# Kernel tuning notes

Hardware: AMD Instinct MI355X
Metric: run time of the kernel (lower is better)

## Reference

```python
import jax, jax.numpy as jnp
import numpy as np

N_NODES = 50000
N_EDGES = 600000
IN_FEATS = 128
N_HIDDEN = 128
N_CLASSES = 40


def setup_inputs() -> dict:
    key = jax.random.key(0)
    ks = jax.random.split(key, 12)
    feat = jax.random.normal(ks[0], (N_NODES, IN_FEATS), dtype=jnp.float32)
    src = jax.random.randint(ks[1], (N_EDGES,), 0, N_NODES, dtype=jnp.int32)
    dst = jax.random.randint(ks[2], (N_EDGES,), 0, N_NODES, dtype=jnp.int32)
    dims = [(IN_FEATS, N_HIDDEN), (N_HIDDEN, N_HIDDEN), (N_HIDDEN, N_CLASSES)]
    params = {}
    for i, (di, do) in enumerate(dims):
        s = 1.0 / np.sqrt(di)
        params[f"w_self{i}"] = jax.random.uniform(ks[3 + 3 * i], (di, do), jnp.float32, -s, s)
        params[f"w_neigh{i}"] = jax.random.uniform(ks[4 + 3 * i], (di, do), jnp.float32, -s, s)
        params[f"b{i}"] = jnp.zeros((do,), jnp.float32)
    return dict(feat=feat, src=src, dst=dst, **params)


def _sage_layer(h, src, dst, w_self, w_neigh, b):
    # mean aggregation over in-neighbors: msg = h[src], reduce at dst
    msg_sum = jax.ops.segment_sum(h[src], dst, num_segments=N_NODES)  # [N, d]
    deg = jax.ops.segment_sum(jnp.ones((src.shape[0],), h.dtype), dst, num_segments=N_NODES)
    h_neigh = msg_sum / jnp.maximum(deg, 1.0)[:, None]
    # DGL SAGEConv(mean): out = fc_self(h) + fc_neigh(mean_neigh) + bias
    return h @ w_self + h_neigh @ w_neigh + b


def reference(feat, src, dst,
              w_self0, w_neigh0, b0,
              w_self1, w_neigh1, b1,
              w_self2, w_neigh2, b2):
    # dropout p=0.0 -> identity
    h = _sage_layer(feat, src, dst, w_self0, w_neigh0, b0)
    h = jax.nn.relu(h)
    h = _sage_layer(h, src, dst, w_self1, w_neigh1, b1)
    h = jax.nn.relu(h)
    h = _sage_layer(h, src, dst, w_self2, w_neigh2, b2)
    return h
```

## Files before the change

kernel.cpp:

```cpp
#include <hip/hip_runtime.h>

#define N_NODES 50000
#define N_EDGES 600000
#define NBLK    196
#define KDIM    128
#define APAD    136

typedef short bf16x8 __attribute__((ext_vector_type(8)));
typedef float f32x4  __attribute__((ext_vector_type(4)));
typedef unsigned short u16x8 __attribute__((ext_vector_type(8)));
typedef unsigned short u16x4 __attribute__((ext_vector_type(4)));

__device__ inline ushort rne_bf16(float a) {
    union { float f; unsigned u; } v; v.f = a;
    return (ushort)((v.u + 0x7FFFu + ((v.u >> 16) & 1u)) >> 16);
}
__device__ inline float bf16_to_f32(ushort h) {
    return __uint_as_float((unsigned)h << 16);
}
__device__ inline void split_bf16(float a, ushort& hi, ushort& lo) {
    hi = rne_bf16(a);
    float hv = bf16_to_f32(hi);
    lo = rne_bf16(a - hv);
}

__global__ __launch_bounds__(256) void k_prep(
    const int* __restrict__ dst, int* __restrict__ degi,
    const float* __restrict__ ws0, const float* __restrict__ wn0,
    const float* __restrict__ ws1, const float* __restrict__ wn1,
    const float* __restrict__ ws2, const float* __restrict__ wn2,
    ushort* __restrict__ Bth0, ushort* __restrict__ Btl0,
    ushort* __restrict__ Bth1, ushort* __restrict__ Btl1,
    ushort* __restrict__ Bth2, ushort* __restrict__ Btl2)
{
    const int b = blockIdx.x, t = threadIdx.x;
    if (b < 192) {
        for (int e = b * 256 + t; e < N_EDGES; e += 192 * 256)
            atomicAdd(&degi[dst[e]], 1);
    } else {
        for (int i = (b - 192) * 256 + t; i < 592 * 128; i += 64 * 256) {
            int bb = i >> 7, k = i & 127;
            const float *Ws, *Wn;
            ushort *H, *L;
            int dout, n;
            if (bb < 256)      { n = bb;       dout = 128; Ws = ws0; Wn = wn0; H = Bth0; L = Btl0; }
            else if (bb < 512) { n = bb - 256; dout = 128; Ws = ws1; Wn = wn1; H = Bth1; L = Btl1; }
            else               { n = bb - 512; dout = 40;  Ws = ws2; Wn = wn2; H = Bth2; L = Btl2; }
            float w = (n < dout) ? Ws[(long)k * dout + n] : Wn[(long)k * dout + (n - dout)];
            ushort hi, lo;
            split_bf16(w, hi, lo);
            H[n * 128 + k] = hi;
            L[n * 128 + k] = lo;
        }
    }
}

__global__ __launch_bounds__(256) void block_sums_kernel(const int* __restrict__ deg,
                                                         int* __restrict__ bsum, int n) {
    __shared__ int s[256];
    int t = threadIdx.x;
    int i = blockIdx.x * 256 + t;
    s[t] = (i < n) ? deg[i] : 0;
    __syncthreads();
    #pragma unroll
    for (int d = 128; d > 0; d >>= 1) {
        if (t < d) s[t] += s[t + d];
        __syncthreads();
    }
    if (t == 0) bsum[blockIdx.x] = s[0];
}

__global__ __launch_bounds__(256) void scatter_fused_kernel(const int* __restrict__ deg,
                                                            const int* __restrict__ bsum,
                                                            int* __restrict__ off,
                                                            int* __restrict__ cur,
                                                            int n, int nb) {
    __shared__ int s[256];
    int t = threadIdx.x;

    int bv = (t < nb) ? bsum[t] : 0;
    s[t] = bv;
    __syncthreads();
    #pragma unroll
    for (int d = 1; d < 256; d <<= 1) {
        int x = (t >= d) ? s[t - d] : 0;
        __syncthreads();
        s[t] += x;
        __syncthreads();
    }
    int base = (blockIdx.x > 0) ? s[blockIdx.x - 1] : 0;
    if (blockIdx.x == 0 && t == 0) off[n] = s[255];
    __syncthreads();

    int i = blockIdx.x * 256 + t;
    int v = (i < n) ? deg[i] : 0;
    s[t] = v;
    __syncthreads();
    #pragma unroll
    for (int d = 1; d < 256; d <<= 1) {
        int x = (t >= d) ? s[t - d] : 0;
        __syncthreads();
        s[t] += x;
        __syncthreads();
    }
    if (i < n) {
        int excl = s[t] - v + base;
        off[i] = excl;
        cur[i] = excl;
    }
}

__device__ __forceinline__ void load_a16(const float* __restrict__ A, int grow, int M, int seg,
                                         float* __restrict__ f) {
    if (grow < M) {
        const float* ap = A + (long)grow * KDIM + seg;
        #pragma unroll
        for (int q = 0; q < 4; ++q) {
            float4 a = *(const float4*)(ap + q * 4);
            f[q * 4 + 0] = a.x; f[q * 4 + 1] = a.y;
            f[q * 4 + 2] = a.z; f[q * 4 + 3] = a.w;
        }
    } else {
        #pragma unroll
        for (int i = 0; i < 16; ++i) f[i] = 0.f;
    }
}

__device__ __forceinline__ void split_store16(const float* __restrict__ f,
                                              ushort* __restrict__ Ahi, ushort* __restrict__ Alo,
                                              int m, int seg) {
    ushort h[16], l[16];
    #pragma unroll
    for (int i = 0; i < 16; ++i) split_bf16(f[i], h[i], l[i]);
    #pragma unroll
    for (int q = 0; q < 2; ++q) {
        uint4 hw, lw;
        hw.x = (unsigned)h[q*8+0] | ((unsigned)h[q*8+1] << 16);
        hw.y = (unsigned)h[q*8+2] | ((unsigned)h[q*8+3] << 16);
        hw.z = (unsigned)h[q*8+4] | ((unsigned)h[q*8+5] << 16);
        hw.w = (unsigned)h[q*8+6] | ((unsigned)h[q*8+7] << 16);
        lw.x = (unsigned)l[q*8+0] | ((unsigned)l[q*8+1] << 16);
        lw.y = (unsigned)l[q*8+2] | ((unsigned)l[q*8+3] << 16);
        lw.z = (unsigned)l[q*8+4] | ((unsigned)l[q*8+5] << 16);
        lw.w = (unsigned)l[q*8+6] | ((unsigned)l[q*8+7] << 16);
        *(uint4*)&Ahi[m * APAD + seg + q * 8] = hw;
        *(uint4*)&Alo[m * APAD + seg + q * 8] = lw;
    }
}

__device__ __forceinline__ void load_pl(const ushort* __restrict__ Phi, const ushort* __restrict__ Plo,
                                        int grow, int M, int seg, uint4* __restrict__ r) {
    if (grow < M) {
        const uint4* ph = (const uint4*)(Phi + (long)grow * KDIM + seg);
        const uint4* pl = (const uint4*)(Plo + (long)grow * KDIM + seg);
        r[0] = ph[0]; r[1] = ph[1];
        r[2] = pl[0]; r[3] = pl[1];
    } else {
        uint4 z = {0, 0, 0, 0};
        r[0] = r[1] = r[2] = r[3] = z;
    }
}

__device__ __forceinline__ void store_pl(const uint4* __restrict__ r,
                                         ushort* __restrict__ Ahi, ushort* __restrict__ Alo,
                                         int m, int seg) {
    *(uint4*)&Ahi[m * APAD + seg] = r[0];
    *(uint4*)&Ahi[m * APAD + seg + 8] = r[1];
    *(uint4*)&Alo[m * APAD + seg] = r[2];
    *(uint4*)&Alo[m * APAD + seg + 8] = r[3];
}

#define WIDE_MFMA_TILE()                                                                      \
    f32x4 acc[2][2] = {};                                                                     \
    _Pragma("unroll")                                                                         \
    for (int c = 0; c < 4; ++c) {                                                             \
        const int k0 = c * 32 + quad * 8;                                                     \
        bf16x8 ah[2], al[2];                                                                  \
        _Pragma("unroll")                                                                     \
        for (int r = 0; r < 2; ++r) {                                                         \
            const int off = (16 * r + lane16) * APAD + k0;                                    \
            ah[r] = *(const bf16x8*)&AH[off];                                                 \
            al[r] = *(const bf16x8*)&AL[off];                                                 \
        }                                                                                     \
        _Pragma("unroll")                                                                     \
        for (int ct = 0; ct < 2; ++ct) {                                                      \
            _Pragma("unroll")                                                                 \
            for (int r = 0; r < 2; ++r) {                                                     \
                acc[r][ct] = __builtin_amdgcn_mfma_f32_16x16x32_bf16(Bh[c][ct], ah[r], acc[r][ct], 0, 0, 0); \
                acc[r][ct] = __builtin_amdgcn_mfma_f32_16x16x32_bf16(Bl[c][ct], ah[r], acc[r][ct], 0, 0, 0); \
                acc[r][ct] = __builtin_amdgcn_mfma_f32_16x16x32_bf16(Bh[c][ct], al[r], acc[r][ct], 0, 0, 0); \
            }                                                                                 \
        }                                                                                     \
    }

#define WIDE_STORE_TILE()                                                                     \
    _Pragma("unroll")                                                                         \
    for (int ct = 0; ct < 2; ++ct) {                                                          \
        const int colL = wave * 32 + 16 * ct + quad * 4;                                      \
        _Pragma("unroll")                                                                     \
        for (int r = 0; r < 2; ++r) {                                                         \
            const int row = rt * 32 + 16 * r + lane16;                                        \
            if (row < M) {                                                                    \
                if (half == 0) {                                                              \
                    *(f32x4*)(S + (long)row * 128 + colL) = acc[r][ct] + bv[ct];              \
                } else {                                                                      \
                    u16x4 t4;                                                                 \
                    _Pragma("unroll")                                                         \
                    for (int i = 0; i < 4; ++i) t4[i] = rne_bf16(acc[r][ct][i]);              \
                    *(u16x4*)(T + (long)row * 128 + colL) = t4;                               \
                }                                                                             \
            }                                                                                 \
        }                                                                                     \
    }

#define WIDE_B_PROLOGUE()                                                                     \
    bf16x8 Bh[4][2], Bl[4][2];                                                                \
    _Pragma("unroll")                                                                         \
    for (int c = 0; c < 4; ++c) {                                                             \
        _Pragma("unroll")                                                                     \
        for (int ct = 0; ct < 2; ++ct) {                                                      \
            const long boff = (long)(colbase + 16 * ct + lane16) * KDIM + c * 32 + quad * 8;  \
            Bh[c][ct] = *(const bf16x8*)(Bth + boff);                                         \
            Bl[c][ct] = *(const bf16x8*)(Btl + boff);                                         \
        }                                                                                     \
    }                                                                                         \
    f32x4 bv[2] = {};                                                                         \
    if (half == 0) {                                                                          \
        _Pragma("unroll")                                                                     \
        for (int ct = 0; ct < 2; ++ct)                                                        \
            bv[ct] = *(const f32x4*)(bias + wave * 32 + 16 * ct + quad * 4);                  \
    }

__global__ __launch_bounds__(256, 3) void k_gemm_wide_f32_fill(
    const float* __restrict__ A,
    const ushort* __restrict__ Bth, const ushort* __restrict__ Btl,
    const float* __restrict__ bias,
    float* __restrict__ S, ushort* __restrict__ T, int M,
    const int* __restrict__ src, const int* __restrict__ dst,
    int* __restrict__ cur, int* __restrict__ ssrcb)
{
    __shared__ ushort AhiB[2][32 * APAD];
    __shared__ ushort AloB[2][32 * APAD];

    if (blockIdx.x < 128) {
        const int gtid = blockIdx.x * 256 + threadIdx.x;
        for (int e = gtid; e < N_EDGES; e += 128 * 256) {
            int p = atomicAdd(&cur[dst[e]], 1);
            ssrcb[p] = src[e];
        }
        return;
    }

    const int bid = blockIdx.x - 128;
    const int tid = threadIdx.x;
    const int wave = tid >> 6;
    const int lane = tid & 63;
    const int lane16 = lane & 15;
    const int quad = lane >> 4;
    const int half = bid & 1;
    const int colbase = half * 128 + wave * 32;
    const int ntiles = (M + 31) >> 5;
    const int bstride = 320;
    const int m   = tid >> 3;
    const int seg = (tid & 7) * 16;

    WIDE_B_PROLOGUE();

    int rt = bid >> 1;
    if (rt >= ntiles) return;

    float fa[16];
    load_a16(A, rt * 32 + m, M, seg, fa);
    split_store16(fa, &AhiB[0][0], &AloB[0][0], m, seg);
    __syncthreads();

    int cur_b = 0;
    while (true) {
        const int nrt = rt + bstride;
        float fn[16];
        if (nrt < ntiles) load_a16(A, nrt * 32 + m, M, seg, fn);

        const ushort* AH = &AhiB[cur_b][0];
        const ushort* AL = &AloB[cur_b][0];

        WIDE_MFMA_TILE();
        WIDE_STORE_TILE();

        if (nrt >= ntiles) break;
        split_store16(fn, &AhiB[cur_b ^ 1][0], &AloB[cur_b ^ 1][0], m, seg);
        __syncthreads();
        cur_b ^= 1;
        rt = nrt;
    }
}

__global__ __launch_bounds__(256, 3) void k_gemm_wide_pl(
    const ushort* __restrict__ Phi, const ushort* __restrict__ Plo,
    const ushort* __restrict__ Bth, const ushort* __restrict__ Btl,
    const float* __restrict__ bias,
    float* __restrict__ S, ushort* __restrict__ T, int M)
{
    __shared__ ushort AhiB[2][32 * APAD];
    __shared__ ushort AloB[2][32 * APAD];

    const int tid = threadIdx.x;
    const int wave = tid >> 6;
    const int lane = tid & 63;
    const int lane16 = lane & 15;
    const int quad = lane >> 4;
    const int half = blockIdx.x & 1;
    const int colbase = half * 128 + wave * 32;
    const int ntiles = (M + 31) >> 5;
    const int bstride = gridDim.x >> 1;
    const int m   = tid >> 3;
    const int seg = (tid & 7) * 16;

    WIDE_B_PROLOGUE();

    int rt = blockIdx.x >> 1;
    if (rt >= ntiles) return;

    uint4 ra[4];
    load_pl(Phi, Plo, rt * 32 + m, M, seg, ra);
    store_pl(ra, &AhiB[0][0], &AloB[0][0], m, seg);
    __syncthreads();

    int cur_b = 0;
    while (true) {
        const int nrt = rt + bstride;
        uint4 rn[4];
        if (nrt < ntiles) load_pl(Phi, Plo, nrt * 32 + m, M, seg, rn);

        const ushort* AH = &AhiB[cur_b][0];
        const ushort* AL = &AloB[cur_b][0];

        WIDE_MFMA_TILE();
        WIDE_STORE_TILE();

        if (nrt >= ntiles) break;
        store_pl(rn, &AhiB[cur_b ^ 1][0], &AloB[cur_b ^ 1][0], m, seg);
        __syncthreads();
        cur_b ^= 1;
        rt = nrt;
    }
}

__global__ __launch_bounds__(256, 2) void k_gemm_narrow_pl(
    const ushort* __restrict__ Phi, const ushort* __restrict__ Plo,
    const ushort* __restrict__ Bth, const ushort* __restrict__ Btl,
    const float* __restrict__ bias,
    float* __restrict__ S, ushort* __restrict__ T, int M)
{
    __shared__ ushort AhiB[2][32 * APAD];
    __shared__ ushort AloB[2][32 * APAD];

    const int tid = threadIdx.x;
    const int wave = tid >> 6;
    const int lane = tid & 63;
    const int lane16 = lane & 15;
    const int quad = lane >> 4;
    const int rtw = wave & 1;
    const int cg = wave >> 1;
    const int ctbase = cg * 3;
    const int nct = cg ? 2 : 3;
    const int ntiles = (M + 31) >> 5;
    const int m   = tid >> 3;
    const int seg = (tid & 7) * 16;

    bf16x8 Bh[4][3], Bl[4][3];
    #pragma unroll
    for (int c = 0; c < 4; ++c) {
        #pragma unroll
        for (int j = 0; j < 3; ++j) {
            if (j < nct) {
                const long boff = (long)(16 * (ctbase + j) + lane16) * KDIM + c * 32 + quad * 8;
                Bh[c][j] = *(const bf16x8*)(Bth + boff);
                Bl[c][j] = *(const bf16x8*)(Btl + boff);
            }
        }
    }

    int rt = blockIdx.x;
    if (rt >= ntiles) return;

    uint4 ra[4];
    load_pl(Phi, Plo, rt * 32 + m, M, seg, ra);
    store_pl(ra, &AhiB[0][0], &AloB[0][0], m, seg);
    __syncthreads();

    int cur_b = 0;
    while (true) {
        const int nrt = rt + gridDim.x;
        uint4 rn[4];
        if (nrt < ntiles) load_pl(Phi, Plo, nrt * 32 + m, M, seg, rn);

        const ushort* AH = &AhiB[cur_b][0];
        const ushort* AL = &AloB[cur_b][0];

        f32x4 acc[3] = {};
        #pragma unroll
        for (int c = 0; c < 4; ++c) {
            const int off = (rtw * 16 + lane16) * APAD + c * 32 + quad * 8;
            bf16x8 ah = *(const bf16x8*)&AH[off];
            bf16x8 al = *(const bf16x8*)&AL[off];
            #pragma unroll
            for (int j = 0; j < 3; ++j) {
                if (j < nct) {
                    acc[j] = __builtin_amdgcn_mfma_f32_16x16x32_bf16(Bh[c][j], ah, acc[j], 0, 0, 0);
                    acc[j] = __builtin_amdgcn_mfma_f32_16x16x32_bf16(Bl[c][j], ah, acc[j], 0, 0, 0);
                    acc[j] = __builtin_amdgcn_mfma_f32_16x16x32_bf16(Bh[c][j], al, acc[j], 0, 0, 0);
                }
            }
        }

        const int row = rt * 32 + rtw * 16 + lane16;
        #pragma unroll
        for (int j = 0; j < 3; ++j) {
            if (j < nct && row < M) {
                const int col0 = 16 * (ctbase + j) + quad * 4;
                if (col0 < 40) {
                    f32x4 bvv = *(const f32x4*)(bias + col0);
                    *(f32x4*)(S + (long)row * 40 + col0) = acc[j] + bvv;
                } else {
                    u16x4 t4;
                    #pragma unroll
                    for (int i = 0; i < 4; ++i) t4[i] = rne_bf16(acc[j][i]);
                    *(u16x4*)(T + (long)row * 40 + (col0 - 40)) = t4;
                }
            }
        }

        if (nrt >= ntiles) break;
        store_pl(rn, &AhiB[cur_b ^ 1][0], &AloB[cur_b ^ 1][0], m, seg);
        __syncthreads();
        cur_b ^= 1;
        rt = nrt;
    }
}

__global__ __launch_bounds__(256) void k_agg128_pl(
    const float* __restrict__ S, const ushort* __restrict__ T,
    const int* __restrict__ off, const int* __restrict__ ssrcb,
    ushort* __restrict__ Phi, ushort* __restrict__ Plo, int nnodes)
{
    const int node = (blockIdx.x * 256 + threadIdx.x) >> 6;
    if (node >= nnodes) return;
    const int lane = threadIdx.x & 63;
    const int slot = lane >> 4;
    const int col8 = (lane & 15) * 8;

    const int a = off[node];
    const int b = off[node + 1];

    f32x4 acc0a = {0,0,0,0}, acc0b = {0,0,0,0};
    f32x4 acc1a = {0,0,0,0}, acc1b = {0,0,0,0};

    int i = a;
    for (; i + 8 <= b; i += 8) {
        int s0 = ssrcb[i + slot];
        int s1 = ssrcb[i + 4 + slot];
        u16x8 v0 = *(const u16x8*)(T + (long)s0 * 128 + col8);
        u16x8 v1 = *(const u16x8*)(T + (long)s1 * 128 + col8);
        #pragma unroll
        for (int j = 0; j < 4; ++j) {
            acc0a[j] += bf16_to_f32(v0[j]);
            acc0b[j] += bf16_to_f32(v0[4 + j]);
            acc1a[j] += bf16_to_f32(v1[j]);
            acc1b[j] += bf16_to_f32(v1[4 + j]);
        }
    }
    for (; i < b; i += 4) {
        int e = i + slot;
        if (e < b) {
            int s = ssrcb[e];
            u16x8 v = *(const u16x8*)(T + (long)s * 128 + col8);
            #pragma unroll
            for (int j = 0; j < 4; ++j) {
                acc0a[j] += bf16_to_f32(v[j]);
                acc0b[j] += bf16_to_f32(v[4 + j]);
            }
        }
    }
    f32x4 accA = acc0a + acc1a;
    f32x4 accB = acc0b + acc1b;

    #pragma unroll
    for (int mm = 16; mm <= 32; mm <<= 1) {
        #pragma unroll
        for (int j = 0; j < 4; ++j) {
            accA[j] += __shfl_xor((float)accA[j], mm);
            accB[j] += __shfl_xor((float)accB[j], mm);
        }
    }

    if (slot == 0) {
        int deg = b - a;
        float scale = (deg > 0) ? (1.0f / (float)deg) : 0.f;
        f32x4 sA = *(const f32x4*)(S + (long)node * 128 + col8);
        f32x4 sB = *(const f32x4*)(S + (long)node * 128 + col8 + 4);
        f32x4 rA = sA + accA * scale;
        f32x4 rB = sB + accB * scale;
        #pragma unroll
        for (int j = 0; j < 4; ++j) {
            rA[j] = fmaxf(rA[j], 0.f);
            rB[j] = fmaxf(rB[j], 0.f);
        }
        u16x8 ph, pl;
        #pragma unroll
        for (int j = 0; j < 4; ++j) {
            ushort h, l;
            split_bf16(rA[j], h, l); ph[j] = h; pl[j] = l;
        }
        #pragma unroll
        for (int j = 0; j < 4; ++j) {
            ushort h, l;
            split_bf16(rB[j], h, l); ph[4 + j] = h; pl[4 + j] = l;
        }
        *(u16x8*)(Phi + (long)node * 128 + col8) = ph;
        *(u16x8*)(Plo + (long)node * 128 + col8) = pl;
    }
}

__global__ __launch_bounds__(256) void k_agg40(
    const float* __restrict__ S, const ushort* __restrict__ T,
    const int* __restrict__ off, const int* __restrict__ ssrcb,
    float* __restrict__ out, int nnodes)
{
    const int node = (blockIdx.x * 256 + threadIdx.x) >> 6;
    if (node >= nnodes) return;
    const int lane = threadIdx.x & 63;
    const bool active = lane < 60;
    const int slot = active ? (lane / 10) : 5;
    const int fi = lane % 10;
    const int fo = fi * 4;

    const int a = off[node];
    const int b = off[node + 1];

    f32x4 acc0 = {0,0,0,0}, acc1 = {0,0,0,0};

    int i = a;
    for (; i + 12 <= b; i += 12) {
        int s0 = ssrcb[i + slot];
        int s1 = ssrcb[i + 6 + slot];
        u16x4 v0 = *(const u16x4*)(T + (long)s0 * 40 + fo);
        u16x4 v1 = *(const u16x4*)(T + (long)s1 * 40 + fo);
        if (active) {
            #pragma unroll
            for (int j = 0; j < 4; ++j) {
                acc0[j] += bf16_to_f32(v0[j]);
                acc1[j] += bf16_to_f32(v1[j]);
            }
        }
    }
    for (; i < b; i += 6) {
        int e = i + slot;
        if (active && e < b) {
            int s = ssrcb[e];
            u16x4 v = *(const u16x4*)(T + (long)s * 40 + fo);
            #pragma unroll
            for (int j = 0; j < 4; ++j) acc0[j] += bf16_to_f32(v[j]);
        }
    }
    f32x4 acc = acc0 + acc1;

    f32x4 tot = acc;
    #pragma unroll
    for (int d = 10; d <= 50; d += 10) {
        int srcl = fi + d;
        #pragma unroll
        for (int j = 0; j < 4; ++j) tot[j] += __shfl((float)acc[j], srcl);
    }

    if (lane < 10) {
        int deg = b - a;
        float scale = (deg > 0) ? (1.0f / (float)deg) : 0.f;
        f32x4 s4 = *(const f32x4*)(S + (long)node * 40 + fo);
        f32x4 r = s4 + tot * scale;
        *(f32x4*)(out + (long)node * 40 + fo) = r;
    }
}


extern "C" void kernel_launch(void* const* d_in, const int* in_sizes, int n_in,
                              void* d_out, int out_size, void* d_ws, size_t ws_size,
                              hipStream_t stream) {
    const float* feat = (const float*)d_in[0];
    const int*   src  = (const int*)d_in[1];
    const int*   dst  = (const int*)d_in[2];
    const float* ws0  = (const float*)d_in[3];
    const float* wn0  = (const float*)d_in[4];
    const float* b0   = (const float*)d_in[5];
    const float* ws1  = (const float*)d_in[6];
    const float* wn1  = (const float*)d_in[7];
    const float* b1   = (const float*)d_in[8];
    const float* ws2  = (const float*)d_in[9];
    const float* wn2  = (const float*)d_in[10];
    const float* b2   = (const float*)d_in[11];

    const int N = N_NODES;

    char* ws = (char*)d_ws;
    int*    offsets = (int*)(ws + 0);
    int*    cursor  = (int*)(ws + 200704);
    int*    degi    = (int*)(ws + 401408);
    int*    bsum    = (int*)(ws + 601600);
    int*    ssrcb   = (int*)(ws + 603648);
    ushort* Phi  = (ushort*)(ws + 3003904);
    ushort* Plo  = (ushort*)(ws + 15803904);
    float*  sbuf = (float*)(ws + 28603904);
    ushort* tbuf = (ushort*)(ws + 54203904);

    ushort* Ball = (ushort*)d_out;
    ushort* Bth0 = Ball;
    ushort* Btl0 = Ball + 32768;
    ushort* Bth1 = Ball + 65536;
    ushort* Btl1 = Ball + 98304;
    ushort* Bth2 = Ball + 131072;
    ushort* Btl2 = Ball + 141312;

    hipMemsetAsync(degi, 0, (size_t)N * sizeof(int), stream);
    k_prep<<<256, 256, 0, stream>>>(dst, degi, ws0, wn0, ws1, wn1, ws2, wn2,
                                    Bth0, Btl0, Bth1, Btl1, Bth2, Btl2);

    block_sums_kernel<<<NBLK, 256, 0, stream>>>(degi, bsum, N);
    scatter_fused_kernel<<<NBLK, 256, 0, stream>>>(degi, bsum, offsets, cursor, N, NBLK);

    const int ga = (N + 3) / 4;

    k_gemm_wide_f32_fill<<<768, 256, 0, stream>>>(feat, Bth0, Btl0, b0, sbuf, tbuf, N,
                                                  src, dst, cursor, ssrcb);
    k_agg128_pl<<<ga, 256, 0, stream>>>(sbuf, tbuf, offsets, ssrcb, Phi, Plo, N);

    k_gemm_wide_pl<<<768, 256, 0, stream>>>(Phi, Plo, Bth1, Btl1, b1, sbuf, tbuf, N);
    k_agg128_pl<<<ga, 256, 0, stream>>>(sbuf, tbuf, offsets, ssrcb, Phi, Plo, N);

    k_gemm_narrow_pl<<<512, 256, 0, stream>>>(Phi, Plo, Bth2, Btl2, b2, sbuf, tbuf, N);
    k_agg40<<<ga, 256, 0, stream>>>(sbuf, tbuf, offsets, ssrcb, (float*)d_out, N);
}
```

Baseline: 275.9 us.

## Drop LDS staging in GEMMs; pre-split input features into bf16 hi/lo in prep

The GEMM kernels no longer stage A tiles through double-buffered shared memory. Each wave now loads its bf16 hi/lo fragments directly from global memory, with the last row clamped for out-of-range tiles. The fp32 input features are split into bf16 hi/lo once in the prep kernel, which grows to 768 blocks, so the first GEMM reads the same hi/lo format as the later layers. This removes LDS traffic, barriers and the in-GEMM split and allows higher occupancy hints. The cost is redundant global or L2 reads across waves that share rows, and an extra pass writing the split features.

```diff
diff --git a/kernel.cpp b/kernel.cpp
--- a/kernel.cpp
+++ b/kernel.cpp
@@ -4,7 +4,6 @@
 #define N_EDGES 600000
 #define NBLK    196
 #define KDIM    128
-#define APAD    136
 
 typedef short bf16x8 __attribute__((ext_vector_type(8)));
 typedef float f32x4  __attribute__((ext_vector_type(4)));
@@ -26,6 +25,8 @@
 
 __global__ __launch_bounds__(256) void k_prep(
     const int* __restrict__ dst, int* __restrict__ degi,
+    const float* __restrict__ feat,
+    ushort* __restrict__ Fhi, ushort* __restrict__ Flo,
     const float* __restrict__ ws0, const float* __restrict__ wn0,
     const float* __restrict__ ws1, const float* __restrict__ wn1,
     const float* __restrict__ ws2, const float* __restrict__ wn2,
@@ -37,7 +38,7 @@
     if (b < 192) {
         for (int e = b * 256 + t; e < N_EDGES; e += 192 * 256)
             atomicAdd(&degi[dst[e]], 1);
-    } else {
+    } else if (b < 256) {
         for (int i = (b - 192) * 256 + t; i < 592 * 128; i += 64 * 256) {
             int bb = i >> 7, k = i & 127;
             const float *Ws, *Wn;
@@ -52,6 +53,35 @@
             H[n * 128 + k] = hi;
             L[n * 128 + k] = lo;
         }
+    } else {
+        for (int idx = (b - 256) * 256 + t; idx < N_NODES * 8; idx += 512 * 256) {
+            const int row = idx >> 3;
+            const int seg = (idx & 7) * 16;
+            const float* ap = feat + (long)row * KDIM + seg;
+            float f[16];
+            #pragma unroll
+            for (int q = 0; q < 4; ++q) {
+                float4 a = *(const float4*)(ap + q * 4);
+                f[q*4+0] = a.x; f[q*4+1] = a.y; f[q*4+2] = a.z; f[q*4+3] = a.w;
+            }
+            ushort h[16], l[16];
+            #pragma unroll
+            for (int i = 0; i < 16; ++i) split_bf16(f[i], h[i], l[i]);
+            #pragma unroll
+            for (int q = 0; q < 2; ++q) {
+                uint4 hw, lw;
+                hw.x = (unsigned)h[q*8+0] | ((unsigned)h[q*8+1] << 16);
+                hw.y = (unsigned)h[q*8+2] | ((unsigned)h[q*8+3] << 16);
+                hw.z = (unsigned)h[q*8+4] | ((unsigned)h[q*8+5] << 16);
+                hw.w = (unsigned)h[q*8+6] | ((unsigned)h[q*8+7] << 16);
+                lw.x = (unsigned)l[q*8+0] | ((unsigned)l[q*8+1] << 16);
+                lw.y = (unsigned)l[q*8+2] | ((unsigned)l[q*8+3] << 16);
+                lw.z = (unsigned)l[q*8+4] | ((unsigned)l[q*8+5] << 16);
+                lw.w = (unsigned)l[q*8+6] | ((unsigned)l[q*8+7] << 16);
+                *(uint4*)&Fhi[(long)row * KDIM + seg + q * 8] = hw;
+                *(uint4*)&Flo[(long)row * KDIM + seg + q * 8] = lw;
+            }
+        }
     }
 }
 
@@ -110,90 +140,47 @@
     }
 }
 
-__device__ __forceinline__ void load_a16(const float* __restrict__ A, int grow, int M, int seg,
-                                         float* __restrict__ f) {
-    if (grow < M) {
-        const float* ap = A + (long)grow * KDIM + seg;
-        #pragma unroll
-        for (int q = 0; q < 4; ++q) {
-            float4 a = *(const float4*)(ap + q * 4);
-            f[q * 4 + 0] = a.x; f[q * 4 + 1] = a.y;
-            f[q * 4 + 2] = a.z; f[q * 4 + 3] = a.w;
-        }
-    } else {
-        #pragma unroll
-        for (int i = 0; i < 16; ++i) f[i] = 0.f;
-    }
-}
-
-__device__ __forceinline__ void split_store16(const float* __restrict__ f,
-                                              ushort* __restrict__ Ahi, ushort* __restrict__ Alo,
-                                              int m, int seg) {
-    ushort h[16], l[16];
-    #pragma unroll
-    for (int i = 0; i < 16; ++i) split_bf16(f[i], h[i], l[i]);
-    #pragma unroll
-    for (int q = 0; q < 2; ++q) {
-        uint4 hw, lw;
-        hw.x = (unsigned)h[q*8+0] | ((unsigned)h[q*8+1] << 16);
-        hw.y = (unsigned)h[q*8+2] | ((unsigned)h[q*8+3] << 16);
-        hw.z = (unsigned)h[q*8+4] | ((unsigned)h[q*8+5] << 16);
-        hw.w = (unsigned)h[q*8+6] | ((unsigned)h[q*8+7] << 16);
-        lw.x = (unsigned)l[q*8+0] | ((unsigned)l[q*8+1] << 16);
-        lw.y = (unsigned)l[q*8+2] | ((unsigned)l[q*8+3] << 16);
-        lw.z = (unsigned)l[q*8+4] | ((unsigned)l[q*8+5] << 16);
-        lw.w = (unsigned)l[q*8+6] | ((unsigned)l[q*8+7] << 16);
-        *(uint4*)&Ahi[m * APAD + seg + q * 8] = hw;
-        *(uint4*)&Alo[m * APAD + seg + q * 8] = lw;
-    }
-}
-
-__device__ __forceinline__ void load_pl(const ushort* __restrict__ Phi, const ushort* __restrict__ Plo,
-                                        int grow, int M, int seg, uint4* __restrict__ r) {
-    if (grow < M) {
-        const uint4* ph = (const uint4*)(Phi + (long)grow * KDIM + seg);
-        const uint4* pl = (const uint4*)(Plo + (long)grow * KDIM + seg);
-        r[0] = ph[0]; r[1] = ph[1];
-        r[2] = pl[0]; r[3] = pl[1];
-    } else {
-        uint4 z = {0, 0, 0, 0};
-        r[0] = r[1] = r[2] = r[3] = z;
-    }
-}
-
-__device__ __forceinline__ void store_pl(const uint4* __restrict__ r,
-                                         ushort* __restrict__ Ahi, ushort* __restrict__ Alo,
-                                         int m, int seg) {
-    *(uint4*)&Ahi[m * APAD + seg] = r[0];
-    *(uint4*)&Ahi[m * APAD + seg + 8] = r[1];
-    *(uint4*)&Alo[m * APAD + seg] = r[2];
-    *(uint4*)&Alo[m * APAD + seg + 8] = r[3];
-}
-
-#define WIDE_MFMA_TILE()                                                                      \
+
+#define WIDE_B_PROLOGUE()                                                                     \
+    bf16x8 Bh[4][2], Bl[4][2];                                                                \
+    _Pragma("unroll")                                                                         \
+    for (int c = 0; c < 4; ++c) {                                                             \
+        _Pragma("unroll")                                                                     \
+        for (int ct = 0; ct < 2; ++ct) {                                                      \
+            const long boff = (long)(colbase + 16 * ct + lane16) * KDIM + c * 32 + quad * 8;  \
+            Bh[c][ct] = *(const bf16x8*)(Bth + boff);                                         \
+            Bl[c][ct] = *(const bf16x8*)(Btl + boff);                                         \
+        }                                                                                     \
+    }                                                                                         \
+    f32x4 bv[2] = {};                                                                         \
+    if (half == 0) {                                                                          \
+        _Pragma("unroll")                                                                     \
+        for (int ct = 0; ct < 2; ++ct)                                                        \
+            bv[ct] = *(const f32x4*)(bias + wave * 32 + 16 * ct + quad * 4);                  \
+    }
+
+#define WIDE_TILE_BODY()                                                                      \
+    const int rr0 = rt * 32 + lane16;                                                         \
+    const int rr1 = rr0 + 16;                                                                 \
+    const long ro0 = (long)((rr0 < M) ? rr0 : (M - 1)) * KDIM + quad * 8;                     \
+    const long ro1 = (long)((rr1 < M) ? rr1 : (M - 1)) * KDIM + quad * 8;                     \
     f32x4 acc[2][2] = {};                                                                     \
     _Pragma("unroll")                                                                         \
     for (int c = 0; c < 4; ++c) {                                                             \
-        const int k0 = c * 32 + quad * 8;                                                     \
-        bf16x8 ah[2], al[2];                                                                  \
-        _Pragma("unroll")                                                                     \
-        for (int r = 0; r < 2; ++r) {                                                         \
-            const int off = (16 * r + lane16) * APAD + k0;                                    \
-            ah[r] = *(const bf16x8*)&AH[off];                                                 \
-            al[r] = *(const bf16x8*)&AL[off];                                                 \
-        }                                                                                     \
+        bf16x8 ah0 = *(const bf16x8*)(Phi + ro0 + c * 32);                                    \
+        bf16x8 al0 = *(const bf16x8*)(Plo + ro0 + c * 32);                                    \
+        bf16x8 ah1 = *(const bf16x8*)(Phi + ro1 + c * 32);                                    \
+        bf16x8 al1 = *(const bf16x8*)(Plo + ro1 + c * 32);                                    \
         _Pragma("unroll")                                                                     \
         for (int ct = 0; ct < 2; ++ct) {                                                      \
-            _Pragma("unroll")                                                                 \
-            for (int r = 0; r < 2; ++r) {                                                     \
-                acc[r][ct] = __builtin_amdgcn_mfma_f32_16x16x32_bf16(Bh[c][ct], ah[r], acc[r][ct], 0, 0, 0); \
-                acc[r][ct] = __builtin_amdgcn_mfma_f32_16x16x32_bf16(Bl[c][ct], ah[r], acc[r][ct], 0, 0, 0); \
-                acc[r][ct] = __builtin_amdgcn_mfma_f32_16x16x32_bf16(Bh[c][ct], al[r], acc[r][ct], 0, 0, 0); \
-            }                                                                                 \
+            acc[0][ct] = __builtin_amdgcn_mfma_f32_16x16x32_bf16(Bh[c][ct], ah0, acc[0][ct], 0, 0, 0); \
+            acc[0][ct] = __builtin_amdgcn_mfma_f32_16x16x32_bf16(Bl[c][ct], ah0, acc[0][ct], 0, 0, 0); \
+            acc[0][ct] = __builtin_amdgcn_mfma_f32_16x16x32_bf16(Bh[c][ct], al0, acc[0][ct], 0, 0, 0); \
+            acc[1][ct] = __builtin_amdgcn_mfma_f32_16x16x32_bf16(Bh[c][ct], ah1, acc[1][ct], 0, 0, 0); \
+            acc[1][ct] = __builtin_amdgcn_mfma_f32_16x16x32_bf16(Bl[c][ct], ah1, acc[1][ct], 0, 0, 0); \
+            acc[1][ct] = __builtin_amdgcn_mfma_f32_16x16x32_bf16(Bh[c][ct], al1, acc[1][ct], 0, 0, 0); \
         }                                                                                     \
-    }
-
-#define WIDE_STORE_TILE()                                                                     \
+    }                                                                                         \
     _Pragma("unroll")                                                                         \
     for (int ct = 0; ct < 2; ++ct) {                                                          \
         const int colL = wave * 32 + 16 * ct + quad * 4;                                      \
@@ -213,35 +200,14 @@
         }                                                                                     \
     }
 
-#define WIDE_B_PROLOGUE()                                                                     \
-    bf16x8 Bh[4][2], Bl[4][2];                                                                \
-    _Pragma("unroll")                                                                         \
-    for (int c = 0; c < 4; ++c) {                                                             \
-        _Pragma("unroll")                                                                     \
-        for (int ct = 0; ct < 2; ++ct) {                                                      \
-            const long boff = (long)(colbase + 16 * ct + lane16) * KDIM + c * 32 + quad * 8;  \
-            Bh[c][ct] = *(const bf16x8*)(Bth + boff);                                         \
-            Bl[c][ct] = *(const bf16x8*)(Btl + boff);                                         \
-        }                                                                                     \
-    }                                                                                         \
-    f32x4 bv[2] = {};                                                                         \
-    if (half == 0) {                                                                          \
-        _Pragma("unroll")                                                                     \
-        for (int ct = 0; ct < 2; ++ct)                                                        \
-            bv[ct] = *(const f32x4*)(bias + wave * 32 + 16 * ct + quad * 4);                  \
-    }
-
-__global__ __launch_bounds__(256, 3) void k_gemm_wide_f32_fill(
-    const float* __restrict__ A,
+__global__ __launch_bounds__(256, 4) void k_gemm_wide_pl_fill(
+    const ushort* __restrict__ Phi, const ushort* __restrict__ Plo,
     const ushort* __restrict__ Bth, const ushort* __restrict__ Btl,
     const float* __restrict__ bias,
     float* __restrict__ S, ushort* __restrict__ T, int M,
     const int* __restrict__ src, const int* __restrict__ dst,
     int* __restrict__ cur, int* __restrict__ ssrcb)
 {
-    __shared__ ushort AhiB[2][32 * APAD];
-    __shared__ ushort AloB[2][32 * APAD];
-
     if (blockIdx.x < 128) {
         const int gtid = blockIdx.x * 256 + threadIdx.x;
         for (int e = gtid; e < N_EDGES; e += 128 * 256) {
@@ -260,49 +226,20 @@
     const int half = bid & 1;
     const int colbase = half * 128 + wave * 32;
     const int ntiles = (M + 31) >> 5;
-    const int bstride = 320;
-    const int m   = tid >> 3;
-    const int seg = (tid & 7) * 16;
 
     WIDE_B_PROLOGUE();
 
-    int rt = bid >> 1;
-    if (rt >= ntiles) return;
-
-    float fa[16];
-    load_a16(A, rt * 32 + m, M, seg, fa);
-    split_store16(fa, &AhiB[0][0], &AloB[0][0], m, seg);
-    __syncthreads();
-
-    int cur_b = 0;
-    while (true) {
-        const int nrt = rt + bstride;
-        float fn[16];
-        if (nrt < ntiles) load_a16(A, nrt * 32 + m, M, seg, fn);
-
-        const ushort* AH = &AhiB[cur_b][0];
-        const ushort* AL = &AloB[cur_b][0];
-
-        WIDE_MFMA_TILE();
-        WIDE_STORE_TILE();
-
-        if (nrt >= ntiles) break;
-        split_store16(fn, &AhiB[cur_b ^ 1][0], &AloB[cur_b ^ 1][0], m, seg);
-        __syncthreads();
-        cur_b ^= 1;
-        rt = nrt;
-    }
-}
-
-__global__ __launch_bounds__(256, 3) void k_gemm_wide_pl(
+    for (int rt = bid >> 1; rt < ntiles; rt += 320) {
+        WIDE_TILE_BODY();
+    }
+}
+
+__global__ __launch_bounds__(256, 4) void k_gemm_wide_pl(
     const ushort* __restrict__ Phi, const ushort* __restrict__ Plo,
     const ushort* __restrict__ Bth, const ushort* __restrict__ Btl,
     const float* __restrict__ bias,
     float* __restrict__ S, ushort* __restrict__ T, int M)
 {
-    __shared__ ushort AhiB[2][32 * APAD];
-    __shared__ ushort AloB[2][32 * APAD];
-
     const int tid = threadIdx.x;
     const int wave = tid >> 6;
     const int lane = tid & 63;
@@ -312,48 +249,20 @@
     const int colbase = half * 128 + wave * 32;
     const int ntiles = (M + 31) >> 5;
     const int bstride = gridDim.x >> 1;
-    const int m   = tid >> 3;
-    const int seg = (tid & 7) * 16;
 
     WIDE_B_PROLOGUE();
 
-    int rt = blockIdx.x >> 1;
-    if (rt >= ntiles) return;
-
-    uint4 ra[4];
-    load_pl(Phi, Plo, rt * 32 + m, M, seg, ra);
-    store_pl(ra, &AhiB[0][0], &AloB[0][0], m, seg);
-    __syncthreads();
-
-    int cur_b = 0;
-    while (true) {
-        const int nrt = rt + bstride;
-        uint4 rn[4];
-        if (nrt < ntiles) load_pl(Phi, Plo, nrt * 32 + m, M, seg, rn);
-
-        const ushort* AH = &AhiB[cur_b][0];
-        const ushort* AL = &AloB[cur_b][0];
-
-        WIDE_MFMA_TILE();
-        WIDE_STORE_TILE();
-
-        if (nrt >= ntiles) break;
-        store_pl(rn, &AhiB[cur_b ^ 1][0], &AloB[cur_b ^ 1][0], m, seg);
-        __syncthreads();
-        cur_b ^= 1;
-        rt = nrt;
-    }
-}
-
-__global__ __launch_bounds__(256, 2) void k_gemm_narrow_pl(
+    for (int rt = blockIdx.x >> 1; rt < ntiles; rt += bstride) {
+        WIDE_TILE_BODY();
+    }
+}
+
+__global__ __launch_bounds__(256, 3) void k_gemm_narrow_pl(
     const ushort* __restrict__ Phi, const ushort* __restrict__ Plo,
     const ushort* __restrict__ Bth, const ushort* __restrict__ Btl,
     const float* __restrict__ bias,
     float* __restrict__ S, ushort* __restrict__ T, int M)
 {
-    __shared__ ushort AhiB[2][32 * APAD];
-    __shared__ ushort AloB[2][32 * APAD];
-
     const int tid = threadIdx.x;
     const int wave = tid >> 6;
     const int lane = tid & 63;
@@ -364,8 +273,6 @@
     const int ctbase = cg * 3;
     const int nct = cg ? 2 : 3;
     const int ntiles = (M + 31) >> 5;
-    const int m   = tid >> 3;
-    const int seg = (tid & 7) * 16;
 
     bf16x8 Bh[4][3], Bl[4][3];
     #pragma unroll
@@ -380,29 +287,15 @@
         }
     }
 
-    int rt = blockIdx.x;
-    if (rt >= ntiles) return;
-
-    uint4 ra[4];
-    load_pl(Phi, Plo, rt * 32 + m, M, seg, ra);
-    store_pl(ra, &AhiB[0][0], &AloB[0][0], m, seg);
-    __syncthreads();
-
-    int cur_b = 0;
-    while (true) {
-        const int nrt = rt + gridDim.x;
-        uint4 rn[4];
-        if (nrt < ntiles) load_pl(Phi, Plo, nrt * 32 + m, M, seg, rn);
-
-        const ushort* AH = &AhiB[cur_b][0];
-        const ushort* AL = &AloB[cur_b][0];
+    for (int rt = blockIdx.x; rt < ntiles; rt += gridDim.x) {
+        const int rr = rt * 32 + rtw * 16 + lane16;
+        const long ro = (long)((rr < M) ? rr : (M - 1)) * KDIM + quad * 8;
 
         f32x4 acc[3] = {};
         #pragma unroll
         for (int c = 0; c < 4; ++c) {
-            const int off = (rtw * 16 + lane16) * APAD + c * 32 + quad * 8;
-            bf16x8 ah = *(const bf16x8*)&AH[off];
-            bf16x8 al = *(const bf16x8*)&AL[off];
+            bf16x8 ah = *(const bf16x8*)(Phi + ro + c * 32);
+            bf16x8 al = *(const bf16x8*)(Plo + ro + c * 32);
             #pragma unroll
             for (int j = 0; j < 3; ++j) {
                 if (j < nct) {
@@ -429,12 +322,6 @@
                 }
             }
         }
-
-        if (nrt >= ntiles) break;
-        store_pl(rn, &AhiB[cur_b ^ 1][0], &AloB[cur_b ^ 1][0], m, seg);
-        __syncthreads();
-        cur_b ^= 1;
-        rt = nrt;
     }
 }
 
@@ -620,7 +507,8 @@
     ushort* Btl2 = Ball + 141312;
 
     hipMemsetAsync(degi, 0, (size_t)N * sizeof(int), stream);
-    k_prep<<<256, 256, 0, stream>>>(dst, degi, ws0, wn0, ws1, wn1, ws2, wn2,
+    k_prep<<<768, 256, 0, stream>>>(dst, degi, feat, Phi, Plo,
+                                    ws0, wn0, ws1, wn1, ws2, wn2,
                                     Bth0, Btl0, Bth1, Btl1, Bth2, Btl2);
 
     block_sums_kernel<<<NBLK, 256, 0, stream>>>(degi, bsum, N);
@@ -628,8 +516,8 @@
 
     const int ga = (N + 3) / 4;
 
-    k_gemm_wide_f32_fill<<<768, 256, 0, stream>>>(feat, Bth0, Btl0, b0, sbuf, tbuf, N,
-                                                  src, dst, cursor, ssrcb);
+    k_gemm_wide_pl_fill<<<768, 256, 0, stream>>>(Phi, Plo, Bth0, Btl0, b0, sbuf, tbuf, N,
+                                                 src, dst, cursor, ssrcb);
     k_agg128_pl<<<ga, 256, 0, stream>>>(sbuf, tbuf, offsets, ssrcb, Phi, Plo, N);
 
     k_gemm_wide_pl<<<768, 256, 0, stream>>>(Phi, Plo, Bth1, Btl1, b1, sbuf, tbuf, N);
```

Result: slower. 302.0 us (+9.4%).

## Use atomic work-stealing tile counters in the three GEMM kernels

Applied to the files above, without the earlier changes.

Replaces the static grid-stride row-tile assignment in the wide and narrow GEMM kernels with dynamic tile fetching from global atomic counters (one per column half), prefetched one tile ahead through a double-buffered shared slot. The goal is to balance load across blocks, especially in the fused fill kernel where edge-scatter blocks compete for the GPU with GEMM blocks. The counters live in workspace and are zeroed by extending the existing memset. The cost is one extra atomic and a shared-memory broadcast per tile, and consecutive tiles may now land on different blocks, which changes cache locality.

```diff
diff --git a/kernel.cpp b/kernel.cpp
--- a/kernel.cpp
+++ b/kernel.cpp
@@ -237,10 +237,12 @@
     const float* __restrict__ bias,
     float* __restrict__ S, ushort* __restrict__ T, int M,
     const int* __restrict__ src, const int* __restrict__ dst,
-    int* __restrict__ cur, int* __restrict__ ssrcb)
+    int* __restrict__ cur, int* __restrict__ ssrcb,
+    int* __restrict__ ctr)
 {
     __shared__ ushort AhiB[2][32 * APAD];
     __shared__ ushort AloB[2][32 * APAD];
+    __shared__ int s_tile[2];
 
     if (blockIdx.x < 128) {
         const int gtid = blockIdx.x * 256 + threadIdx.x;
@@ -260,37 +262,42 @@
     const int half = bid & 1;
     const int colbase = half * 128 + wave * 32;
     const int ntiles = (M + 31) >> 5;
-    const int bstride = 320;
     const int m   = tid >> 3;
     const int seg = (tid & 7) * 16;
+    int* myctr = ctr + half;
 
     WIDE_B_PROLOGUE();
 
-    int rt = bid >> 1;
+    if (tid == 0) s_tile[0] = atomicAdd(myctr, 1);
+    __syncthreads();
+    int rt = s_tile[0];
     if (rt >= ntiles) return;
 
     float fa[16];
     load_a16(A, rt * 32 + m, M, seg, fa);
     split_store16(fa, &AhiB[0][0], &AloB[0][0], m, seg);
-    __syncthreads();
-
-    int cur_b = 0;
+    if (tid == 0) s_tile[1] = atomicAdd(myctr, 1);
+    __syncthreads();
+    int nrt = s_tile[1];
+
+    int sp = 0, cur_b = 0;
     while (true) {
-        const int nrt = rt + bstride;
         float fn[16];
         if (nrt < ntiles) load_a16(A, nrt * 32 + m, M, seg, fn);
 
         const ushort* AH = &AhiB[cur_b][0];
         const ushort* AL = &AloB[cur_b][0];
-
         WIDE_MFMA_TILE();
         WIDE_STORE_TILE();
 
         if (nrt >= ntiles) break;
+        if (tid == 0) s_tile[sp] = atomicAdd(myctr, 1);
         split_store16(fn, &AhiB[cur_b ^ 1][0], &AloB[cur_b ^ 1][0], m, seg);
         __syncthreads();
+        rt = nrt;
+        nrt = s_tile[sp];
+        sp ^= 1;
         cur_b ^= 1;
-        rt = nrt;
     }
 }
 
@@ -298,10 +305,12 @@
     const ushort* __restrict__ Phi, const ushort* __restrict__ Plo,
     const ushort* __restrict__ Bth, const ushort* __restrict__ Btl,
     const float* __restrict__ bias,
-    float* __restrict__ S, ushort* __restrict__ T, int M)
+    float* __restrict__ S, ushort* __restrict__ T, int M,
+    int* __restrict__ ctr)
 {
     __shared__ ushort AhiB[2][32 * APAD];
     __shared__ ushort AloB[2][32 * APAD];
+    __shared__ int s_tile[2];
 
     const int tid = threadIdx.x;
     const int wave = tid >> 6;
@@ -311,37 +320,42 @@
     const int half = blockIdx.x & 1;
     const int colbase = half * 128 + wave * 32;
     const int ntiles = (M + 31) >> 5;
-    const int bstride = gridDim.x >> 1;
     const int m   = tid >> 3;
     const int seg = (tid & 7) * 16;
+    int* myctr = ctr + half;
 
     WIDE_B_PROLOGUE();
 
-    int rt = blockIdx.x >> 1;
+    if (tid == 0) s_tile[0] = atomicAdd(myctr, 1);
+    __syncthreads();
+    int rt = s_tile[0];
     if (rt >= ntiles) return;
 
     uint4 ra[4];
     load_pl(Phi, Plo, rt * 32 + m, M, seg, ra);
     store_pl(ra, &AhiB[0][0], &AloB[0][0], m, seg);
-    __syncthreads();
-
-    int cur_b = 0;
+    if (tid == 0) s_tile[1] = atomicAdd(myctr, 1);
+    __syncthreads();
+    int nrt = s_tile[1];
+
+    int sp = 0, cur_b = 0;
     while (true) {
-        const int nrt = rt + bstride;
         uint4 rn[4];
         if (nrt < ntiles) load_pl(Phi, Plo, nrt * 32 + m, M, seg, rn);
 
         const ushort* AH = &AhiB[cur_b][0];
         const ushort* AL = &AloB[cur_b][0];
-
         WIDE_MFMA_TILE();
         WIDE_STORE_TILE();
 
         if (nrt >= ntiles) break;
+        if (tid == 0) s_tile[sp] = atomicAdd(myctr, 1);
         store_pl(rn, &AhiB[cur_b ^ 1][0], &AloB[cur_b ^ 1][0], m, seg);
         __syncthreads();
+        rt = nrt;
+        nrt = s_tile[sp];
+        sp ^= 1;
         cur_b ^= 1;
-        rt = nrt;
     }
 }
 
@@ -349,10 +363,12 @@
     const ushort* __restrict__ Phi, const ushort* __restrict__ Plo,
     const ushort* __restrict__ Bth, const ushort* __restrict__ Btl,
     const float* __restrict__ bias,
-    float* __restrict__ S, ushort* __restrict__ T, int M)
+    float* __restrict__ S, ushort* __restrict__ T, int M,
+    int* __restrict__ ctr)
 {
     __shared__ ushort AhiB[2][32 * APAD];
     __shared__ ushort AloB[2][32 * APAD];
+    __shared__ int s_tile[2];
 
     const int tid = threadIdx.x;
     const int wave = tid >> 6;
@@ -380,17 +396,20 @@
         }
     }
 
-    int rt = blockIdx.x;
+    if (tid == 0) s_tile[0] = atomicAdd(ctr, 1);
+    __syncthreads();
+    int rt = s_tile[0];
     if (rt >= ntiles) return;
 
     uint4 ra[4];
     load_pl(Phi, Plo, rt * 32 + m, M, seg, ra);
     store_pl(ra, &AhiB[0][0], &AloB[0][0], m, seg);
-    __syncthreads();
-
-    int cur_b = 0;
+    if (tid == 0) s_tile[1] = atomicAdd(ctr, 1);
+    __syncthreads();
+    int nrt = s_tile[1];
+
+    int sp = 0, cur_b = 0;
     while (true) {
-        const int nrt = rt + gridDim.x;
         uint4 rn[4];
         if (nrt < ntiles) load_pl(Phi, Plo, nrt * 32 + m, M, seg, rn);
 
@@ -431,10 +450,13 @@
         }
 
         if (nrt >= ntiles) break;
+        if (tid == 0) s_tile[sp] = atomicAdd(ctr, 1);
         store_pl(rn, &AhiB[cur_b ^ 1][0], &AloB[cur_b ^ 1][0], m, seg);
         __syncthreads();
+        rt = nrt;
+        nrt = s_tile[sp];
+        sp ^= 1;
         cur_b ^= 1;
-        rt = nrt;
     }
 }
 
@@ -604,6 +626,7 @@
     int*    offsets = (int*)(ws + 0);
     int*    cursor  = (int*)(ws + 200704);
     int*    degi    = (int*)(ws + 401408);
+    int*    tctr    = (int*)(ws + 601408);
     int*    bsum    = (int*)(ws + 601600);
     int*    ssrcb   = (int*)(ws + 603648);
     ushort* Phi  = (ushort*)(ws + 3003904);
@@ -619,7 +642,7 @@
     ushort* Bth2 = Ball + 131072;
     ushort* Btl2 = Ball + 141312;
 
-    hipMemsetAsync(degi, 0, (size_t)N * sizeof(int), stream);
+    hipMemsetAsync(degi, 0, (size_t)N * sizeof(int) + 64, stream);
     k_prep<<<256, 256, 0, stream>>>(dst, degi, ws0, wn0, ws1, wn1, ws2, wn2,
                                     Bth0, Btl0, Bth1, Btl1, Bth2, Btl2);
 
@@ -629,12 +652,12 @@
     const int ga = (N + 3) / 4;
 
     k_gemm_wide_f32_fill<<<768, 256, 0, stream>>>(feat, Bth0, Btl0, b0, sbuf, tbuf, N,
-                                                  src, dst, cursor, ssrcb);
+                                                  src, dst, cursor, ssrcb, tctr);
     k_agg128_pl<<<ga, 256, 0, stream>>>(sbuf, tbuf, offsets, ssrcb, Phi, Plo, N);
 
-    k_gemm_wide_pl<<<768, 256, 0, stream>>>(Phi, Plo, Bth1, Btl1, b1, sbuf, tbuf, N);
+    k_gemm_wide_pl<<<768, 256, 0, stream>>>(Phi, Plo, Bth1, Btl1, b1, sbuf, tbuf, N, tctr + 2);
     k_agg128_pl<<<ga, 256, 0, stream>>>(sbuf, tbuf, offsets, ssrcb, Phi, Plo, N);
 
-    k_gemm_narrow_pl<<<512, 256, 0, stream>>>(Phi, Plo, Bth2, Btl2, b2, sbuf, tbuf, N);
+    k_gemm_narrow_pl<<<512, 256, 0, stream>>>(Phi, Plo, Bth2, Btl2, b2, sbuf, tbuf, N, tctr + 4);
     k_agg40<<<ga, 256, 0, stream>>>(sbuf, tbuf, offsets, ssrcb, (float*)d_out, N);
 }
```

Result: slower. 353.4 us (+28.1%).

## Stage GEMM A tiles via async global-to-LDS loads with XOR-swizzled layout

Applied to the files above, without the earlier changes.

The two bf16-pair GEMM kernels now copy each 32-row A tile straight from global memory into LDS with global_load_lds. This replaces the old path that loaded the tile into registers and then wrote it to padded LDS, removing the register round trip and the separate store step. The LDS tile is now unpadded (128 wide), so the aggregation kernel writes its hi/lo outputs with an XOR column swizzle keyed on the node index, and the GEMM reads use the matching swizzled offsets to avoid bank conflicts. The tail tile no longer zero-fills rows beyond M, so it may read past the end of the Phi/Plo buffers. The global-memory layout of the intermediate activations also changes to the swizzled order.

```diff
diff --git a/kernel.cpp b/kernel.cpp
--- a/kernel.cpp
+++ b/kernel.cpp
@@ -148,26 +148,21 @@
     }
 }
 
-__device__ __forceinline__ void load_pl(const ushort* __restrict__ Phi, const ushort* __restrict__ Plo,
-                                        int grow, int M, int seg, uint4* __restrict__ r) {
-    if (grow < M) {
-        const uint4* ph = (const uint4*)(Phi + (long)grow * KDIM + seg);
-        const uint4* pl = (const uint4*)(Plo + (long)grow * KDIM + seg);
-        r[0] = ph[0]; r[1] = ph[1];
-        r[2] = pl[0]; r[3] = pl[1];
-    } else {
-        uint4 z = {0, 0, 0, 0};
-        r[0] = r[1] = r[2] = r[3] = z;
-    }
-}
-
-__device__ __forceinline__ void store_pl(const uint4* __restrict__ r,
-                                         ushort* __restrict__ Ahi, ushort* __restrict__ Alo,
-                                         int m, int seg) {
-    *(uint4*)&Ahi[m * APAD + seg] = r[0];
-    *(uint4*)&Ahi[m * APAD + seg + 8] = r[1];
-    *(uint4*)&Alo[m * APAD + seg] = r[2];
-    *(uint4*)&Alo[m * APAD + seg + 8] = r[3];
+__device__ __forceinline__ void stage_pl_async(const ushort* __restrict__ Phi,
+                                               const ushort* __restrict__ Plo,
+                                               int tilebase, int wave, int lane,
+                                               ushort* lds16k) {
+    const char* gsrc = (wave < 2)
+        ? (const char*)(Phi + (long)tilebase * KDIM) + wave * 4096
+        : (const char*)(Plo + (long)tilebase * KDIM) + (wave - 2) * 4096;
+    char* ldst = (char*)lds16k + wave * 4096;
+    #pragma unroll
+    for (int j = 0; j < 4; ++j) {
+        __builtin_amdgcn_global_load_lds(
+            (const __attribute__((address_space(1))) unsigned int*)(const void*)(gsrc + j * 1024 + lane * 16),
+            (__attribute__((address_space(3))) unsigned int*)(void*)(ldst + j * 1024),
+            16, 0, 0);
+    }
 }
 
 #define WIDE_MFMA_TILE()                                                                      \
@@ -193,6 +188,29 @@
         }                                                                                     \
     }
 
+#define WIDE_MFMA_TILE_SW()                                                                   \
+    f32x4 acc[2][2] = {};                                                                     \
+    _Pragma("unroll")                                                                         \
+    for (int c = 0; c < 4; ++c) {                                                             \
+        bf16x8 ah[2], al[2];                                                                  \
+        _Pragma("unroll")                                                                     \
+        for (int r = 0; r < 2; ++r) {                                                         \
+            const int p = (quad + 4 * c) ^ (lane16 & 7);                                      \
+            const int off = (16 * r + lane16) * 128 + p * 8;                                  \
+            ah[r] = *(const bf16x8*)&AH[off];                                                 \
+            al[r] = *(const bf16x8*)&AL[off];                                                 \
+        }                                                                                     \
+        _Pragma("unroll")                                                                     \
+        for (int ct = 0; ct < 2; ++ct) {                                                      \
+            _Pragma("unroll")                                                                 \
+            for (int r = 0; r < 2; ++r) {                                                     \
+                acc[r][ct] = __builtin_amdgcn_mfma_f32_16x16x32_bf16(Bh[c][ct], ah[r], acc[r][ct], 0, 0, 0); \
+                acc[r][ct] = __builtin_amdgcn_mfma_f32_16x16x32_bf16(Bl[c][ct], ah[r], acc[r][ct], 0, 0, 0); \
+                acc[r][ct] = __builtin_amdgcn_mfma_f32_16x16x32_bf16(Bh[c][ct], al[r], acc[r][ct], 0, 0, 0); \
+            }                                                                                 \
+        }                                                                                     \
+    }
+
 #define WIDE_STORE_TILE()                                                                     \
     _Pragma("unroll")                                                                         \
     for (int ct = 0; ct < 2; ++ct) {                                                          \
@@ -282,7 +300,6 @@
 
         const ushort* AH = &AhiB[cur_b][0];
         const ushort* AL = &AloB[cur_b][0];
-
         WIDE_MFMA_TILE();
         WIDE_STORE_TILE();
 
@@ -300,8 +317,7 @@
     const float* __restrict__ bias,
     float* __restrict__ S, ushort* __restrict__ T, int M)
 {
-    __shared__ ushort AhiB[2][32 * APAD];
-    __shared__ ushort AloB[2][32 * APAD];
+    __shared__ ushort AB[2][8192];
 
     const int tid = threadIdx.x;
     const int wave = tid >> 6;
@@ -312,33 +328,27 @@
     const int colbase = half * 128 + wave * 32;
     const int ntiles = (M + 31) >> 5;
     const int bstride = gridDim.x >> 1;
-    const int m   = tid >> 3;
-    const int seg = (tid & 7) * 16;
 
     WIDE_B_PROLOGUE();
 
     int rt = blockIdx.x >> 1;
     if (rt >= ntiles) return;
 
-    uint4 ra[4];
-    load_pl(Phi, Plo, rt * 32 + m, M, seg, ra);
-    store_pl(ra, &AhiB[0][0], &AloB[0][0], m, seg);
+    stage_pl_async(Phi, Plo, rt * 32, wave, lane, &AB[0][0]);
     __syncthreads();
 
     int cur_b = 0;
     while (true) {
         const int nrt = rt + bstride;
-        uint4 rn[4];
-        if (nrt < ntiles) load_pl(Phi, Plo, nrt * 32 + m, M, seg, rn);
-
-        const ushort* AH = &AhiB[cur_b][0];
-        const ushort* AL = &AloB[cur_b][0];
-
-        WIDE_MFMA_TILE();
+        if (nrt < ntiles)
+            stage_pl_async(Phi, Plo, nrt * 32, wave, lane, &AB[cur_b ^ 1][0]);
+
+        const ushort* AH = &AB[cur_b][0];
+        const ushort* AL = AH + 4096;
+        WIDE_MFMA_TILE_SW();
         WIDE_STORE_TILE();
 
         if (nrt >= ntiles) break;
-        store_pl(rn, &AhiB[cur_b ^ 1][0], &AloB[cur_b ^ 1][0], m, seg);
         __syncthreads();
         cur_b ^= 1;
         rt = nrt;
@@ -351,8 +361,7 @@
     const float* __restrict__ bias,
     float* __restrict__ S, ushort* __restrict__ T, int M)
 {
-    __shared__ ushort AhiB[2][32 * APAD];
-    __shared__ ushort AloB[2][32 * APAD];
+    __shared__ ushort AB[2][8192];
 
     const int tid = threadIdx.x;
     const int wave = tid >> 6;
@@ -364,8 +373,6 @@
     const int ctbase = cg * 3;
     const int nct = cg ? 2 : 3;
     const int ntiles = (M + 31) >> 5;
-    const int m   = tid >> 3;
-    const int seg = (tid & 7) * 16;
 
     bf16x8 Bh[4][3], Bl[4][3];
     #pragma unroll
@@ -383,24 +390,23 @@
     int rt = blockIdx.x;
     if (rt >= ntiles) return;
 
-    uint4 ra[4];
-    load_pl(Phi, Plo, rt * 32 + m, M, seg, ra);
-    store_pl(ra, &AhiB[0][0], &AloB[0][0], m, seg);
+    stage_pl_async(Phi, Plo, rt * 32, wave, lane, &AB[0][0]);
     __syncthreads();
 
     int cur_b = 0;
     while (true) {
         const int nrt = rt + gridDim.x;
-        uint4 rn[4];
-        if (nrt < ntiles) load_pl(Phi, Plo, nrt * 32 + m, M, seg, rn);
-
-        const ushort* AH = &AhiB[cur_b][0];
-        const ushort* AL = &AloB[cur_b][0];
+        if (nrt < ntiles)
+            stage_pl_async(Phi, Plo, nrt * 32, wave, lane, &AB[cur_b ^ 1][0]);
+
+        const ushort* AH = &AB[cur_b][0];
+        const ushort* AL = AH + 4096;
 
         f32x4 acc[3] = {};
         #pragma unroll
         for (int c = 0; c < 4; ++c) {
-            const int off = (rtw * 16 + lane16) * APAD + c * 32 + quad * 8;
+            const int p = (quad + 4 * c) ^ (lane16 & 7);
+            const int off = (rtw * 16 + lane16) * 128 + p * 8;
             bf16x8 ah = *(const bf16x8*)&AH[off];
             bf16x8 al = *(const bf16x8*)&AL[off];
             #pragma unroll
@@ -431,7 +437,6 @@
         }
 
         if (nrt >= ntiles) break;
-        store_pl(rn, &AhiB[cur_b ^ 1][0], &AloB[cur_b ^ 1][0], m, seg);
         __syncthreads();
         cur_b ^= 1;
         rt = nrt;
@@ -516,8 +521,9 @@
             ushort h, l;
             split_bf16(rB[j], h, l); ph[4 + j] = h; pl[4 + j] = l;
         }
-        *(u16x8*)(Phi + (long)node * 128 + col8) = ph;
-        *(u16x8*)(Plo + (long)node * 128 + col8) = pl;
+        const int colsw = (((lane & 15) ^ (node & 7)) * 8);
+        *(u16x8*)(Phi + (long)node * 128 + colsw) = ph;
+        *(u16x8*)(Plo + (long)node * 128 + colsw) = pl;
     }
 }
 
```

Measured after the change: 276.1 us. About the same (+0.1%).
